# Optimization experiments

Hardware: AMD Instinct MI355X
Metric: run time of the kernel (lower is better)

## Reference

```python
import jax, jax.numpy as jnp
import numpy as np

LSTM = 256
NUM_CELLS = 5
BLOCKS = 6
TEMP = 5.0
TANH_C = 1.1


def setup_inputs() -> dict:
    key = jax.random.key(0)
    ks = jax.random.split(key, 8)
    s = 0.05  # small init so sigmoids/tanh stay in sane range
    return {
        "enc_w": jax.random.normal(ks[0], (5, LSTM), jnp.float32) * s,
        "w_ih": jax.random.normal(ks[1], (4 * LSTM, LSTM), jnp.float32) * s,
        "w_hh": jax.random.normal(ks[2], (4 * LSTM, LSTM), jnp.float32) * s,
        "b_ih": jax.random.normal(ks[3], (4 * LSTM,), jnp.float32) * s,
        "b_hh": jax.random.normal(ks[4], (4 * LSTM,), jnp.float32) * s,
        "w1": jax.random.normal(ks[5], (LSTM, LSTM), jnp.float32) * s,
        "w2": jax.random.normal(ks[6], (LSTM, LSTM), jnp.float32) * s,
        "v": jax.random.normal(ks[7], (LSTM,), jnp.float32) * s,
    }


def _lstm_cell(x, h, c, w_ih, w_hh, b_ih, b_hh):
    # torch.nn.LSTMCell gate order: i, f, g, o
    g = w_ih @ x + b_ih + w_hh @ h + b_hh  # [4*LSTM]
    i, f, gg, o = jnp.split(g, 4)
    i, f, o = jax.nn.sigmoid(i), jax.nn.sigmoid(f), jax.nn.sigmoid(o)
    c2 = f * c + i * jnp.tanh(gg)
    h2 = o * jnp.tanh(c2)
    return h2, c2


def _run_sampler(bkey, enc_w, w_ih, w_hh, b_ih, b_hh, w1, w2, v):
    zeros = jnp.zeros((LSTM,), jnp.float32)
    inputs = enc_w[0]  # encoder(0)
    anchors = []
    anchors_w1 = []
    prev_h = prev_c = zeros
    # first two layers: LSTM always fed zero state (faithful to source)
    for _ in range(2):
        prev_h, prev_c = _lstm_cell(inputs, zeros, zeros, w_ih, w_hh, b_ih, b_hh)
        anchors.append(zeros)
        anchors_w1.append(w1 @ prev_h)
    arc_seq, log_probs, entropies = [], [], []
    step = 0
    for layer_id in range(2, NUM_CELLS + 2):
        for _ in range(2):
            prev_h, prev_c = _lstm_cell(inputs, prev_h, prev_c, w_ih, w_hh, b_ih, b_hh)
            q = jnp.tanh(jnp.stack(anchors_w1[:layer_id]) + w2 @ prev_h)  # [layer_id, LSTM]
            logits = (q @ v) / TEMP  # [layer_id]
            logits = TANH_C * jnp.tanh(logits)
            skey = jax.random.fold_in(bkey, step); step += 1
            index = jax.random.categorical(skey, logits)
            lsm = jax.nn.log_softmax(logits)
            arc_seq.append(index)
            log_probs.append(-lsm[index])  # F.cross_entropy
            entropies.append(jax.lax.stop_gradient(-jnp.sum(lsm * jnp.exp(lsm))))
            inputs = jnp.stack(anchors[:layer_id])[index]
        prev_h, prev_c = _lstm_cell(inputs, prev_h, prev_c, w_ih, w_hh, b_ih, b_hh)
        anchors.append(prev_h)
        anchors_w1.append(w1 @ prev_h)
        inputs = enc_w[0]
    arc = jnp.stack(arc_seq)  # [2*NUM_CELLS] int
    return arc, sum(entropies), sum(log_probs), prev_c, prev_h


def reference(enc_w, w_ih, w_hh, b_ih, b_hh, w1, w2, v):
    key = jax.random.key(42)
    all_arc = []
    all_entropy = jnp.float32(0.0)
    all_log_prob = jnp.float32(0.0)
    c = h = None
    for b in range(BLOCKS):
        arc, ent, lp, c, h = _run_sampler(
            jax.random.fold_in(key, b), enc_w, w_ih, w_hh, b_ih, b_hh, w1, w2, v)
        all_arc.append(arc)
        all_entropy = all_entropy + ent
        all_log_prob = all_log_prob + lp
    return (jnp.stack(all_arc), all_log_prob, all_entropy, c[None, :], h[None, :])
```

## Files before the change

### kernel.cpp

```cpp
#include <hip/hip_runtime.h>
#include <stdint.h>


#define NBLK  6
#define PWG   8
#define THR   512
#define TINYF 1.17549435e-38f
#define HTAGB 0xC3B00000u
#define YTAGB 0xE1700000u
#define DONE_MAGIC 0x444f4e45

typedef unsigned long long u64;
struct U2 { uint32_t x, y; };

#define W_DONE 0u
#define W_PART 64u
#define W_HX   128u
#define W_YMB  24704u
#define W_NEED 221312u

#define S_READY 0u
#define S_DONE  192u
#define S_PART  224u
#define S_HP    320u
#define S_ACC   24896u
#define FXS     67108864.0f
#define READY_MAGIC 0x52454459

__device__ __forceinline__ U2 tf2x32(uint32_t k0, uint32_t k1,
                                     uint32_t c0, uint32_t c1) {
  uint32_t ks2 = k0 ^ k1 ^ 0x1BD11BDAu;
  uint32_t x0 = c0 + k0, x1 = c1 + k1;
#define TFR(r) { x0 += x1; x1 = (x1 << (r)) | (x1 >> (32 - (r))); x1 ^= x0; }
  TFR(13) TFR(15) TFR(26) TFR(6)   x0 += k1;  x1 += ks2 + 1u;
  TFR(17) TFR(29) TFR(16) TFR(24)  x0 += ks2; x1 += k0 + 2u;
  TFR(13) TFR(15) TFR(26) TFR(6)   x0 += k0;  x1 += k1 + 3u;
  TFR(17) TFR(29) TFR(16) TFR(24)  x0 += k1;  x1 += ks2 + 4u;
  TFR(13) TFR(15) TFR(26) TFR(6)   x0 += ks2; x1 += k0 + 5u;
#undef TFR
  U2 r; r.x = x0; r.y = x1; return r;
}

__device__ __forceinline__ float sigf(float x) {
  return 1.0f / (1.0f + expf(-x));
}
__device__ __forceinline__ void istore(int* p, int v) {
  __hip_atomic_store(p, v, __ATOMIC_RELAXED, __HIP_MEMORY_SCOPE_AGENT);
}
__device__ __forceinline__ int iload(const int* p) {
  return __hip_atomic_load(p, __ATOMIC_RELAXED, __HIP_MEMORY_SCOPE_AGENT);
}
__device__ __forceinline__ void hstore(u64* p, u64 v) {
  __hip_atomic_store(p, v, __ATOMIC_RELAXED, __HIP_MEMORY_SCOPE_AGENT);
}
__device__ __forceinline__ u64 hload(const u64* p) {
  return __hip_atomic_load(p, __ATOMIC_RELAXED, __HIP_MEMORY_SCOPE_AGENT);
}
__device__ __forceinline__ void fstore(float* p, float v) {
  __hip_atomic_store(p, v, __ATOMIC_RELAXED, __HIP_MEMORY_SCOPE_AGENT);
}
__device__ __forceinline__ float fload(const float* p) {
  return __hip_atomic_load(p, __ATOMIC_RELAXED, __HIP_MEMORY_SCOPE_AGENT);
}
__device__ __forceinline__ u64 pollw(const u64* p, uint32_t want) {
  u64 v;
  for (;;) {
    v = hload(p);
    if ((uint32_t)(v >> 32) == want) return v;
    __builtin_amdgcn_s_sleep(1);
  }
}

__global__ __launch_bounds__(THR, 1) void ctrl_v12(
    const float* __restrict__ enc_w,
    const float* __restrict__ wih,
    const float* __restrict__ whh,
    const float* __restrict__ b_ih,
    const float* __restrict__ b_hh,
    const float* __restrict__ w1,
    const float* __restrict__ w2,
    const float* __restrict__ vvec,
    unsigned char* __restrict__ ws,
    float* __restrict__ out) {

  const int b = blockIdx.x & 7;
  const int p = blockIdx.x >> 3;
  if (b >= NBLK) return;
  const int tid = threadIdx.x;

  int*   done = (int*)(ws + W_DONE);
  float* part = (float*)(ws + W_PART);
  u64*   hx   = (u64*)(ws + W_HX);
  u64*   ymb  = (u64*)(ws + W_YMB);

  const int r4 = tid >> 2, s4 = tid & 3;
  const int grow = (r4 >> 5) * 256 + p * 32 + (r4 & 31);
  const int k0 = s4 * 64;
  const int rr = tid & 255, ks = tid >> 8;
  const int cb = p * 32 + ks * 16;

  __shared__ __align__(16) float gateL[THR];
  __shared__ __align__(16) float hL[256], encL[256], vL[256];
  __shared__ __align__(16) float anchL[4][256];
  __shared__ __align__(16) float w2hS[256], aw1S[6][256];
  __shared__ float rowSumL[128], biasS[128], h2S[32];
  __shared__ float logitL[8];
  __shared__ int   selL;

  if (tid < 256) { encL[tid] = enc_w[tid]; vL[tid] = vvec[tid]; }
  if (tid < 128) {
    int r = (tid >> 5) * 256 + p * 32 + (tid & 31);
    biasS[tid] = b_ih[r] + b_hh[r];
  }

  float4 wihr[16], whhr[16];
  #pragma unroll
  for (int c = 0; c < 16; ++c) {
    wihr[c] = *(const float4*)(wih + grow * 256 + k0 + c * 4);
    whhr[c] = *(const float4*)(whh + grow * 256 + k0 + c * 4);
  }
  float w1c[16], w2c[16];
  #pragma unroll
  for (int j = 0; j < 16; ++j) {
    w1c[j] = w1[rr * 256 + cb + j];
    w2c[j] = w2[rr * 256 + cb + j];
  }
  __syncthreads();

  auto dotIH = [&](const float* x) {
    float a = 0.0f;
    #pragma unroll
    for (int c = 0; c < 16; ++c) {
      float4 xv = *(const float4*)(x + k0 + c * 4);
      float4 w = wihr[c];
      a += w.x * xv.x + w.y * xv.y + w.z * xv.z + w.w * xv.w;
    }
    return a;
  };
  auto dotHH = [&]() {
    float a = 0.0f;
    #pragma unroll
    for (int c = 0; c < 16; ++c) {
      float4 xv = *(const float4*)(hL + k0 + c * 4);
      float4 w = whhr[c];
      a += w.x * xv.x + w.y * xv.y + w.z * xv.z + w.w * xv.w;
    }
    return a;
  };

  const float encih = dotIH(encL);

  float cv = 0.0f;
  U2 bk = tf2x32(0u, 42u, 0u, (uint32_t)b);
  int k = 1, step = 0;
  float lpAcc = 0.0f, entAcc = 0.0f;

  auto cell = [&](float gacc, int mode, int aid, int cid) {
    float a1 = __shfl_xor(gacc, 1);
    float a2 = __shfl_xor(gacc, 2);
    float a3 = __shfl_xor(gacc, 3);
    if (s4 == 0) rowSumL[r4] = ((gacc + a1) + a2) + a3 + biasS[r4];
    __syncthreads();
    if (tid < 32) {
      float gi = rowSumL[tid],       gf = rowSumL[32 + tid];
      float gg2 = rowSumL[64 + tid], go = rowSumL[96 + tid];
      float c2 = sigf(gf) * cv + sigf(gi) * tanhf(gg2);
      float h2 = sigf(go) * tanhf(c2);
      cv = c2;
      h2S[tid] = h2;
      if (mode == 2) {
        if (b == NBLK - 1) { out[62 + p * 32 + tid] = cv; out[318 + p * 32 + tid] = h2; }
      } else {
        hstore(&hx[(k & 1) * 1536 + b * 256 + p * 32 + tid],
               ((u64)(HTAGB | (uint32_t)k) << 32) | (u64)__float_as_uint(h2));
      }
    }
    __syncthreads();
    if (mode == 2) return;

    {
      const float* wc = (mode == 1) ? w1c : w2c;
      float yp = 0.0f;
      #pragma unroll
      for (int j = 0; j < 16; ++j) yp += wc[j] * h2S[ks * 16 + j];
      gateL[tid] = yp;
    }
    __syncthreads();

    const uint32_t wantY = YTAGB | (uint32_t)k;
    const uint32_t wantH = HTAGB | (uint32_t)k;
    u64* yslot = ymb + (size_t)(k & 1) * 12288 + (size_t)b * 2048;
    if (tid < 256) {
      float yp2 = gateL[tid] + gateL[256 + tid];
      hstore(yslot + p * 256 + tid,
             ((u64)wantY << 32) | (u64)__float_as_uint(yp2));
      u64 v = pollw(&hx[(k & 1) * 1536 + b * 256 + tid], wantH);
      float hv = __uint_as_float((uint32_t)v);
      hL[tid] = hv;
      if (mode == 1 && cid >= 0) anchL[cid][tid] = hv;
    } else {
      const int e = tid & 255;
      const u64* bp = yslot + e;
      u64 w[8];
      for (;;) {
        bool ok = true;
        #pragma unroll
        for (int q = 0; q < 8; ++q) {
          w[q] = hload(bp + q * 256);
          ok &= ((uint32_t)(w[q] >> 32) == wantY);
        }
        if (ok) break;
        __builtin_amdgcn_s_sleep(1);
      }
      float y = 0.0f;
      #pragma unroll
      for (int q = 0; q < 8; ++q) y += __uint_as_float((uint32_t)w[q]);
      if (mode == 1) aw1S[aid][e] = y; else w2hS[e] = y;
    }
    __syncthreads();
    ++k;
  };

  auto resolve = [&](int L) -> int {
    int wv = tid >> 6, lane = tid & 63;
    if (wv < L) {
      float a = 0.0f;
      #pragma unroll
      for (int j = 0; j < 4; ++j) {
        int kk = j * 64 + lane;
        a += tanhf(aw1S[wv][kk] + w2hS[kk]) * vL[kk];
      }
      a += __shfl_down(a, 32);
      a += __shfl_down(a, 16);
      a += __shfl_down(a, 8);
      a += __shfl_down(a, 4);
      a += __shfl_down(a, 2);
      a += __shfl_down(a, 1);
      if (lane == 0) logitL[wv] = a;
    }
    __syncthreads();
    if (tid < 64) {
      float lg = 0.0f, sgum = -1e30f;
      if (tid < L) {
        lg = 1.1f * tanhf(logitL[tid] * 0.2f);
        U2 sk = tf2x32(bk.x, bk.y, 0u, (uint32_t)step);
        U2 r2 = tf2x32(sk.x, sk.y, 0u, (uint32_t)tid);
        uint32_t bits = r2.x ^ r2.y;
        float u = __uint_as_float((bits >> 9) | 0x3f800000u) - 1.0f;
        u = fmaxf(TINYF, u + TINYF);
        sgum = lg - logf(-logf(u));
      }
      int bi = 0;
      float best = __shfl(sgum, 0, 64);
      for (int j = 1; j < L; ++j) {
        float sj = __shfl(sgum, j, 64);
        if (sj > best) { best = sj; bi = j; }
      }
      float mx = __shfl(lg, 0, 64);
      for (int j = 1; j < L; ++j) mx = fmaxf(mx, __shfl(lg, j, 64));
      float se = 0.0f;
      for (int j = 0; j < L; ++j) se += expf(__shfl(lg, j, 64) - mx);
      float lse = logf(se);
      float lgbi = __shfl(lg, bi, 64);
      float es = 0.0f;
      for (int j = 0; j < L; ++j) {
        float l = __shfl(lg, j, 64) - mx - lse;
        es += l * expf(l);
      }
      if (tid == 0) {
        lpAcc += -(lgbi - mx - lse);
        entAcc += -es;
        selL = bi;
        if (p == 0) out[b * 10 + step] = (float)bi;
      }
    }
    __syncthreads();
    step++;
    return selL;
  };

  cell(encih, 1, 0, -1);
  if (tid < 256) aw1S[1][tid] = aw1S[0][tid];
  __syncthreads();

  for (int L = 2; L <= 6; ++L) {
    { float hh = dotHH(); cell(encih + hh, 0, 0, -1); }
    {
      float hh = dotHH();
      int s1 = resolve(L);
      float a = (s1 >= 2) ? dotIH(&anchL[s1 - 2][0]) : 0.0f;
      cell(a + hh, 0, 0, -1);
    }
    {
      float hh = dotHH();
      int s2 = resolve(L);
      float a = (s2 >= 2) ? dotIH(&anchL[s2 - 2][0]) : 0.0f;
      if (L < 6) cell(a + hh, 1, L, L - 2);
      else       cell(a + hh, 2, 0, -1);
    }
  }

  if (p == 0 && tid == 0) {
    fstore(&part[2 * b], lpAcc);
    fstore(&part[2 * b + 1], entAcc);
    __builtin_amdgcn_s_waitcnt(0);
    istore(&done[b], DONE_MAGIC);
    if (b == NBLK - 1) {
      float lp = 0.0f, en = 0.0f;
      for (int j = 0; j < NBLK; ++j) {
        while (iload(&done[j]) != DONE_MAGIC) __builtin_amdgcn_s_sleep(1);
        lp += fload(&part[2 * j]);
        en += fload(&part[2 * j + 1]);
      }
      out[60] = lp;
      out[61] = en;
    }
  }
}

__global__ __launch_bounds__(1024) void ctrl_small(
    const float* __restrict__ enc_w,
    const float* __restrict__ wih,
    const float* __restrict__ whh,
    const float* __restrict__ b_ih,
    const float* __restrict__ b_hh,
    const float* __restrict__ w1,
    const float* __restrict__ w2,
    const float* __restrict__ vvec,
    unsigned char* __restrict__ ws,
    float* __restrict__ out) {

  const int b = blockIdx.x & 7;
  const int p = blockIdx.x >> 3;
  if (b >= NBLK) return;
  const int tid = threadIdx.x;

  int*   ready = (int*)(ws + S_READY);
  int*   done  = (int*)(ws + S_DONE);
  float* part  = (float*)(ws + S_PART);
  u64*   hp    = (u64*)(ws + S_HP);
  int*   acc   = (int*)(ws + S_ACC);

  const int rl = tid >> 3, s = tid & 7;
  const int g = rl >> 5, el = rl & 31;
  const int row = g * 256 + p * 32 + el;
  const int k0 = s * 32;
  const int rr = tid & 255, ks = tid >> 8;

  __shared__ __align__(16) float hL[256], encL[256], vL[256];
  __shared__ __align__(16) float anchL[4][256];
  __shared__ __align__(16) float partL[1024];
  __shared__ __align__(16) float w2hS[256], aw1S[6][256];
  __shared__ float rowSumL[128], biasS[128], h2S[32];
  __shared__ float logitL[8];
  __shared__ int   selL;

  if (tid < 256) { encL[tid] = enc_w[tid]; vL[tid] = vvec[tid]; }
  if (tid < 128) {
    int gg = tid >> 5, ee = tid & 31, r = gg * 256 + p * 32 + ee;
    biasS[tid] = b_ih[r] + b_hh[r];
  }

  float4 wihr[8], whhr[8];
  #pragma unroll
  for (int c = 0; c < 8; ++c) {
    int cc = (c + s) & 7;
    wihr[c] = *(const float4*)(wih + row * 256 + k0 + cc * 4);
    whhr[c] = *(const float4*)(whh + row * 256 + k0 + cc * 4);
  }
  float w1c[8], w2c[8];
  #pragma unroll
  for (int j = 0; j < 8; ++j) {
    w1c[j] = w1[rr * 256 + p * 32 + ks * 8 + j];
    w2c[j] = w2[rr * 256 + p * 32 + ks * 8 + j];
  }

  if (tid < 32) istore(&acc[1 * (NBLK * 256) + b * 256 + p * 32 + tid], 0);
  __syncthreads();
  if (tid == 0) istore(&ready[b * 8 + p], READY_MAGIC);
  if (tid < 8) {
    while (iload(&ready[b * 8 + tid]) != READY_MAGIC)
      __builtin_amdgcn_s_sleep(1);
  }
  __syncthreads();

  auto dotIH = [&](const float* x) {
    float a = 0.0f;
    #pragma unroll
    for (int c = 0; c < 8; ++c) {
      int cc = (c + s) & 7;
      float4 xv = *(const float4*)(x + k0 + cc * 4);
      float4 w = wihr[c];
      a += w.x * xv.x + w.y * xv.y + w.z * xv.z + w.w * xv.w;
    }
    return a;
  };
  auto dotHH = [&]() {
    float a = 0.0f;
    #pragma unroll
    for (int c = 0; c < 8; ++c) {
      int cc = (c + s) & 7;
      float4 xv = *(const float4*)(hL + k0 + cc * 4);
      float4 w = whhr[c];
      a += w.x * xv.x + w.y * xv.y + w.z * xv.z + w.w * xv.w;
    }
    return a;
  };

  const float encih = dotIH(encL);
  float cv = 0.0f;
  U2 bk = tf2x32(0u, 42u, 0u, (uint32_t)b);
  int k = 1, step = 0;
  float lpAcc = 0.0f, entAcc = 0.0f;

  auto cell = [&](float gacc, int mode, int aid, int cid) {
    partL[tid] = gacc;
    __syncthreads();
    if (tid < 128) {
      float ssum = 0.0f;
      #pragma unroll
      for (int j = 0; j < 8; ++j) ssum += partL[tid * 8 + j];
      rowSumL[tid] = ssum + biasS[tid];
    }
    __syncthreads();
    if (tid < 32) {
      float gi = rowSumL[tid],       gf = rowSumL[32 + tid];
      float gg2 = rowSumL[64 + tid], go = rowSumL[96 + tid];
      float c2 = sigf(gf) * cv + sigf(gi) * tanhf(gg2);
      float h2 = sigf(go) * tanhf(c2);
      cv = c2;
      h2S[tid] = h2;
      if (mode == 2 && b == NBLK - 1) {
        out[62 + p * 32 + tid] = cv;
        out[318 + p * 32 + tid] = h2;
      }
    }
    __syncthreads();
    if (mode == 2) return;
    {
      const float* wc = (mode == 1) ? w1c : w2c;
      float yp = 0.0f;
      #pragma unroll
      for (int j = 0; j < 8; ++j) yp += wc[j] * h2S[ks * 8 + j];
      atomicAdd(&acc[(k % 3) * (NBLK * 256) + b * 256 + rr],
                __float2int_rn(yp * FXS));
      if (tid < 32)
        istore(&acc[((k + 1) % 3) * (NBLK * 256) + b * 256 + p * 32 + tid], 0);
    }
    __syncthreads();
    if (tid < 32) {
      u64 pk = ((u64)(uint32_t)k << 32) | (u64)__float_as_uint(h2S[tid]);
      hstore(&hp[(k & 1) * (NBLK * 256) + b * 256 + p * 32 + tid], pk);
    }
    if (tid < 256) {
      u64 v;
      const u64* src = &hp[(k & 1) * (NBLK * 256) + b * 256 + tid];
      while ((int)(hload(src) >> 32) != k) __builtin_amdgcn_s_sleep(1);
      v = hload(src);
      float hv = __uint_as_float((uint32_t)v);
      hL[tid] = hv;
      if (mode == 1 && cid >= 0) anchL[cid][tid] = hv;
    }
    __syncthreads();
    if (tid < 256) {
      int iv = iload(&acc[(k % 3) * (NBLK * 256) + b * 256 + tid]);
      float f = (float)((double)iv * (1.0 / 67108864.0));
      if (mode == 1) aw1S[aid][tid] = f; else w2hS[tid] = f;
    }
    __syncthreads();
    ++k;
  };

  auto sample = [&](int L) -> int {
    int wv = tid >> 6, lane = tid & 63;
    if (wv < L) {
      float a = 0.0f;
      #pragma unroll
      for (int j = 0; j < 4; ++j) {
        int kk = lane * 4 + j;
        a += tanhf(aw1S[wv][kk] + w2hS[kk]) * vL[kk];
      }
      a += __shfl_down(a, 32);
      a += __shfl_down(a, 16);
      a += __shfl_down(a, 8);
      a += __shfl_down(a, 4);
      a += __shfl_down(a, 2);
      a += __shfl_down(a, 1);
      if (lane == 0) logitL[wv] = a;
    }
    __syncthreads();
    if (tid < 64) {
      float lg = 0.0f, sgum = -1e30f;
      if (tid < L) {
        lg = 1.1f * tanhf(logitL[tid] * 0.2f);
        U2 sk = tf2x32(bk.x, bk.y, 0u, (uint32_t)step);
        U2 r2 = tf2x32(sk.x, sk.y, 0u, (uint32_t)tid);
        uint32_t bits = r2.x ^ r2.y;
        float u = __uint_as_float((bits >> 9) | 0x3f800000u) - 1.0f;
        u = fmaxf(TINYF, u + TINYF);
        sgum = lg - logf(-logf(u));
      }
      int bi = 0;
      float best = __shfl(sgum, 0, 64);
      for (int j = 1; j < L; ++j) {
        float sj = __shfl(sgum, j, 64);
        if (sj > best) { best = sj; bi = j; }
      }
      float mx = __shfl(lg, 0, 64);
      for (int j = 1; j < L; ++j) mx = fmaxf(mx, __shfl(lg, j, 64));
      float se = 0.0f;
      for (int j = 0; j < L; ++j) se += expf(__shfl(lg, j, 64) - mx);
      float lse = logf(se);
      float lgbi = __shfl(lg, bi, 64);
      float es = 0.0f;
      for (int j = 0; j < L; ++j) {
        float l = __shfl(lg, j, 64) - mx - lse;
        es += l * expf(l);
      }
      if (tid == 0) {
        lpAcc += -(lgbi - mx - lse);
        entAcc += -es;
        selL = bi;
        if (p == 0) out[b * 10 + step] = (float)bi;
      }
    }
    __syncthreads();
    step++;
    return selL;
  };

  cell(encih, 1, 0, -1);
  if (tid < 256) aw1S[1][tid] = aw1S[0][tid];
  __syncthreads();
  for (int L = 2; L <= 6; ++L) {
    cell(encih + dotHH(), 0, 0, -1);
    int s1v = sample(L);
    {
      float a = (s1v >= 2) ? dotIH(&anchL[s1v - 2][0]) : 0.0f;
      cell(a + dotHH(), 0, 0, -1);
    }
    int s2v = sample(L);
    {
      float a = (s2v >= 2) ? dotIH(&anchL[s2v - 2][0]) : 0.0f;
      if (L < 6) cell(a + dotHH(), 1, L, L - 2);
      else       cell(a + dotHH(), 2, 0, -1);
    }
  }
  if (p == 0 && tid == 0) {
    fstore(&part[2 * b], lpAcc);
    fstore(&part[2 * b + 1], entAcc);
    __builtin_amdgcn_s_waitcnt(0);
    istore(&done[b], DONE_MAGIC);
    if (b == NBLK - 1) {
      float lp = 0.0f, en = 0.0f;
      for (int j = 0; j < NBLK; ++j) {
        while (iload(&done[j]) != DONE_MAGIC) __builtin_amdgcn_s_sleep(1);
        lp += fload(&part[2 * j]);
        en += fload(&part[2 * j + 1]);
      }
      out[60] = lp;
      out[61] = en;
    }
  }
}

extern "C" void kernel_launch(void* const* d_in, const int* in_sizes, int n_in,
                              void* d_out, int out_size, void* d_ws, size_t ws_size,
                              hipStream_t stream) {
  const float* enc = (const float*)d_in[0];
  const float* wih = (const float*)d_in[1];
  const float* whh = (const float*)d_in[2];
  const float* bih = (const float*)d_in[3];
  const float* bhh = (const float*)d_in[4];
  const float* w1  = (const float*)d_in[5];
  const float* w2  = (const float*)d_in[6];
  const float* v   = (const float*)d_in[7];
  unsigned char* ws = (unsigned char*)d_ws;
  float* out = (float*)d_out;

  if (ws_size >= W_NEED) {
    ctrl_v12<<<dim3(64), dim3(THR), 0, stream>>>(
        enc, wih, whh, bih, bhh, w1, w2, v, ws, out);
  } else {
    ctrl_small<<<dim3(64), dim3(1024), 0, stream>>>(
        enc, wih, whh, bih, bhh, w1, w2, v, ws, out);
  }
}
```

Measured before the change: 175.1 us.

## Reorganize gate reduction via LDS and poll peer partials incrementally

Threads now map rows across the four K-slices (tid&127 with slice tid>>7) instead of putting them in adjacent lanes, so the per-row gate reduction goes through shared memory with an extra barrier rather than lane shuffles. In the cross-workgroup exchange, each workgroup uses its own partial straight from LDS and only polls peers it has not yet received, which cuts redundant global loads while waiting. Launch bounds change to allow two blocks per CU, which may limit registers for the large per-thread weight arrays.

```diff
diff --git a/kernel.cpp b/kernel.cpp
--- a/kernel.cpp
+++ b/kernel.cpp
@@ -71,7 +71,7 @@
   }
 }
 
-__global__ __launch_bounds__(THR, 1) void ctrl_v12(
+__global__ __launch_bounds__(THR, 2) void ctrl_v13(
     const float* __restrict__ enc_w,
     const float* __restrict__ wih,
     const float* __restrict__ whh,
@@ -93,9 +93,9 @@
   u64*   hx   = (u64*)(ws + W_HX);
   u64*   ymb  = (u64*)(ws + W_YMB);
 
-  const int r4 = tid >> 2, s4 = tid & 3;
-  const int grow = (r4 >> 5) * 256 + p * 32 + (r4 & 31);
-  const int k0 = s4 * 64;
+  const int rl = tid & 127, s = tid >> 7;
+  const int grow = (rl >> 5) * 256 + p * 32 + (rl & 31);
+  const int k0 = s * 64;
   const int rr = tid & 255, ks = tid >> 8;
   const int cb = p * 32 + ks * 16;
 
@@ -156,10 +156,14 @@
   float lpAcc = 0.0f, entAcc = 0.0f;
 
   auto cell = [&](float gacc, int mode, int aid, int cid) {
-    float a1 = __shfl_xor(gacc, 1);
-    float a2 = __shfl_xor(gacc, 2);
-    float a3 = __shfl_xor(gacc, 3);
-    if (s4 == 0) rowSumL[r4] = ((gacc + a1) + a2) + a3 + biasS[r4];
+    gateL[tid] = gacc;
+    __syncthreads();
+    if (tid < 128) {
+      float ssum = 0.0f;
+      #pragma unroll
+      for (int j = 0; j < 4; ++j) ssum += gateL[j * 128 + tid];
+      rowSumL[tid] = ssum + biasS[tid];
+    }
     __syncthreads();
     if (tid < 32) {
       float gi = rowSumL[tid],       gf = rowSumL[32 + tid];
@@ -199,22 +203,33 @@
       hL[tid] = hv;
       if (mode == 1 && cid >= 0) anchL[cid][tid] = hv;
     } else {
-      const int e = tid & 255;
+      const int e = tid - 256;
       const u64* bp = yslot + e;
-      u64 w[8];
+      float own = gateL[e] + gateL[256 + e];
+      float ys[8];
+      unsigned got = 1u << p;
+      #pragma unroll
+      for (int q = 0; q < 8; ++q) ys[q] = (q == p) ? own : 0.0f;
       for (;;) {
-        bool ok = true;
+        bool all = true;
         #pragma unroll
         for (int q = 0; q < 8; ++q) {
-          w[q] = hload(bp + q * 256);
-          ok &= ((uint32_t)(w[q] >> 32) == wantY);
+          if (!(got & (1u << q))) {
+            u64 w = hload(bp + q * 256);
+            if ((uint32_t)(w >> 32) == wantY) {
+              ys[q] = __uint_as_float((uint32_t)w);
+              got |= 1u << q;
+            } else {
+              all = false;
+            }
+          }
         }
-        if (ok) break;
+        if (all) break;
         __builtin_amdgcn_s_sleep(1);
       }
       float y = 0.0f;
       #pragma unroll
-      for (int q = 0; q < 8; ++q) y += __uint_as_float((uint32_t)w[q]);
+      for (int q = 0; q < 8; ++q) y += ys[q];
       if (mode == 1) aw1S[aid][e] = y; else w2hS[e] = y;
     }
     __syncthreads();
@@ -579,7 +594,7 @@
   float* out = (float*)d_out;
 
   if (ws_size >= W_NEED) {
-    ctrl_v12<<<dim3(64), dim3(THR), 0, stream>>>(
+    ctrl_v13<<<dim3(64), dim3(THR), 0, stream>>>(
         enc, wih, whh, bih, bhh, w1, w2, v, ws, out);
   } else {
     ctrl_small<<<dim3(64), dim3(1024), 0, stream>>>(
```

After: 161.4 us. 7.8% less time.
